# Kernel tuning notes

Measured on AMD Instinct MI355X. Metric: run time of the kernel, lower is better.

## Reference

```python
import jax, jax.numpy as jnp
import numpy as np
from jax import lax

B = 1024
D_VQ = 64
KS = 1024
KX = 1024
BETA = 0.25


def _conv1d(x, w, b):
    # x: [N, Cin, L], w: [Cout, Cin, 3], 'same' padding
    y = lax.conv_general_dilated(x, w, (1,), [(1, 1)], dimension_numbers=('NCH', 'OIH', 'NCH'))
    return y + b[None, :, None]


def _conv2d(x, w, b):
    # x: [N, Cin, H, W], w: [Cout, Cin, 3, 3], 'same' padding
    y = lax.conv_general_dilated(x, w, (1, 1), [(1, 1), (1, 1)], dimension_numbers=('NCHW', 'OIHW', 'NCHW'))
    return y + b[None, :, None, None]


def _gelu(x):
    return jax.nn.gelu(x, approximate=False)


def _vq_ema(z_e, codebook, beta):
    # z_e: [N, D], codebook: [K, D]
    d = (jnp.sum(z_e * z_e, axis=1, keepdims=True)
         - 2.0 * (z_e @ codebook.T)
         + jnp.sum(codebook * codebook, axis=1)[None, :])  # [N, K]
    idx = jnp.argmin(d, axis=1)                              # [N]
    z_q = codebook[idx]                                      # gather [N, D]
    vq_loss = beta * jnp.mean((z_e - lax.stop_gradient(z_q)) ** 2)
    z_q_st = z_e + lax.stop_gradient(z_q - z_e)              # straight-through
    n = z_e.shape[0]
    probs = jnp.zeros((codebook.shape[0],), z_e.dtype).at[idx].add(1.0) / n
    perplexity = jnp.exp(-jnp.sum(probs * jnp.log(probs + 1e-10)))
    return z_q_st, idx, vq_loss, perplexity


def setup_inputs() -> dict:
    key = jax.random.key(0)
    ks = iter(jax.random.split(key, 40))

    def p(shape, s=0.05):
        return jax.random.normal(next(ks), shape, jnp.float32) * s

    inp = {
        'cubes': jax.random.normal(next(ks), (B, 9, 8, 72), jnp.float32),
        # spectral encoder
        's_w1': p((16, 1, 3)), 's_b1': jnp.zeros((16,), jnp.float32),
        's_w2': p((16, 16, 3)), 's_b2': jnp.zeros((16,), jnp.float32),
        's_fc_w': p((D_VQ, 16 * 8)), 's_fc_b': jnp.zeros((D_VQ,), jnp.float32),
        'cb_s': p((KS, D_VQ), 1.0),
        # spectral decoder
        's_dec_fc_w': p((16 * 8, D_VQ)), 's_dec_fc_b': jnp.zeros((16 * 8,), jnp.float32),
        's_dec_w1': p((16, 16, 3)), 's_dec_b1': jnp.zeros((16,), jnp.float32),
        's_dec_w2': p((1, 16, 3)), 's_dec_b2': jnp.zeros((1,), jnp.float32),
        # spatial encoder
        'x_w1': p((16, 8, 3, 3)), 'x_b1': jnp.zeros((16,), jnp.float32),
        'x_w2': p((16, 16, 3, 3)), 'x_b2': jnp.zeros((16,), jnp.float32),
        'x_fc_w': p((D_VQ, 16 * 3 * 3)), 'x_fc_b': jnp.zeros((D_VQ,), jnp.float32),
        'cb_x': p((KX, D_VQ), 1.0),
        # spatial decoder
        'x_dec_fc_w': p((16 * 3 * 3, D_VQ)), 'x_dec_fc_b': jnp.zeros((16 * 3 * 3,), jnp.float32),
        'x_dec_w1': p((16, 16, 3, 3)), 'x_dec_b1': jnp.zeros((16,), jnp.float32),
        'x_dec_w2': p((8, 16, 3, 3)), 'x_dec_b2': jnp.zeros((8,), jnp.float32),
        'return_recon': 1,
    }
    return inp


def reference(cubes, s_w1, s_b1, s_w2, s_b2, s_fc_w, s_fc_b, cb_s,
              s_dec_fc_w, s_dec_fc_b, s_dec_w1, s_dec_b1, s_dec_w2, s_dec_b2,
              x_w1, x_b1, x_w2, x_b2, x_fc_w, x_fc_b, cb_x,
              x_dec_fc_w, x_dec_fc_b, x_dec_w1, x_dec_b1, x_dec_w2, x_dec_b2,
              return_recon):
    b, p, t, f = cubes.shape
    n = b * p * t
    c6 = cubes.reshape(b, p, t, 8, 3, 3)                   # [B,P,T,8,3,3]
    cperm = jnp.transpose(c6, (0, 1, 2, 4, 5, 3))          # [B,P,T,3,3,8]

    # --- spectral path ---
    spec = jnp.mean(cperm, axis=(3, 4))                    # [B,P,T,8]
    spec_seq = spec.reshape(n, 1, 8)
    s = _gelu(_conv1d(spec_seq, s_w1, s_b1))
    s = _gelu(_conv1d(s, s_w2, s_b2))
    z_e_s = s.reshape(n, 16 * 8) @ s_fc_w.T + s_fc_b       # [N,D]
    z_q_s, k_idx, vq_loss_s, perplex_s = _vq_ema(z_e_s, cb_s, BETA)
    emb_s = z_q_s.reshape(b, p, t, D_VQ)
    k_idx = k_idx.reshape(b, p, t)

    # --- spatial path ---
    spatial = c6.reshape(n, 8, 3, 3)
    x = _gelu(_conv2d(spatial, x_w1, x_b1))
    x = _gelu(_conv2d(x, x_w2, x_b2))
    z_e_x = x.reshape(n, 16 * 9) @ x_fc_w.T + x_fc_b
    z_q_x, m_idx, vq_loss_x, perplex_x = _vq_ema(z_e_x, cb_x, BETA)
    emb_x = z_q_x.reshape(b, p, t, D_VQ)
    m_idx = m_idx.reshape(b, p, t)

    total = vq_loss_s + vq_loss_x

    if return_recon:
        s_dec = (z_q_s @ s_dec_fc_w.T + s_dec_fc_b).reshape(n, 16, 8)
        s_dec = _gelu(_conv1d(s_dec, s_dec_w1, s_dec_b1))
        recon_s = _conv1d(s_dec, s_dec_w2, s_dec_b2)[:, 0, :].reshape(b, p, t, 8)
        recon_loss_s = jnp.mean((recon_s - spec) ** 2)

        x_dec = (z_q_x @ x_dec_fc_w.T + x_dec_fc_b).reshape(n, 16, 3, 3)
        x_dec = _gelu(_conv2d(x_dec, x_dec_w1, x_dec_b1))
        recon_x = _conv2d(x_dec, x_dec_w2, x_dec_b2)        # [N,8,3,3]
        recon_loss_x = jnp.mean((recon_x - spatial) ** 2)
        recon_loss_total = recon_loss_s + recon_loss_x
    else:
        recon_loss_total = jnp.float32(0.0)

    return (emb_s, emb_x, k_idx, m_idx, total, perplex_s, perplex_x, recon_loss_total)
```

## Files before the change

### kernel.cpp

```cpp
#include <hip/hip_runtime.h>
#include <math.h>

#define NTOK 73728

__device__ __forceinline__ float gelu_f(float x) {
    return 0.5f * x * (1.0f + erff(x * 0.70710678118654752440f));
}

__global__ void __launch_bounds__(256) k_prep(
    const float* __restrict__ cb_s, const float* __restrict__ cb_x,
    double* __restrict__ cn_s, double* __restrict__ cn_x,
    const float* __restrict__ s_dw1, const float* __restrict__ s_db1,
    const float* __restrict__ s_dfcw, const float* __restrict__ s_dfcb,
    float* __restrict__ weffT_s, float* __restrict__ beff_s,
    const float* __restrict__ x_dw1, const float* __restrict__ x_db1,
    const float* __restrict__ x_dfcw, const float* __restrict__ x_dfcb,
    float* __restrict__ weffT_x, float* __restrict__ beff_x,
    const float* __restrict__ s_fcw, float* __restrict__ fcwT_s,
    const float* __restrict__ x_fcw, float* __restrict__ fcwT_x,
    const float* __restrict__ s_w2, float* __restrict__ sw2T,
    const float* __restrict__ x_w1, float* __restrict__ xw1T,
    const float* __restrict__ x_w2, float* __restrict__ xw2T,
    const float* __restrict__ x_dw2, float* __restrict__ xdw2T)
{
    int bid = blockIdx.x, tid = threadIdx.x;
    if (bid < 8) {
        int i = bid * 256 + tid;
        const float* cb = (i < 1024) ? cb_s : cb_x;
        double* cn = (i < 1024) ? cn_s : cn_x;
        int c = i & 1023;
        double s = 0.0;
        for (int k = 0; k < 64; ++k) { double v = (double)cb[c * 64 + k]; s += v * v; }
        cn[c] = s;
    } else if (bid < 40) {
        int idx = (bid - 8) * 256 + tid;
        int o = idx >> 6, d = idx & 63;
        int c = o >> 3, l = o & 7;
        double acc = 0.0;
        for (int ci = 0; ci < 16; ++ci)
            for (int dd = 0; dd < 3; ++dd) {
                int ll = l + dd - 1;
                if (ll < 0 || ll > 7) continue;
                acc += (double)s_dw1[(c * 16 + ci) * 3 + dd] * (double)s_dfcw[(ci * 8 + ll) * 64 + d];
            }
        weffT_s[d * 132 + o] = (float)acc;
        if (o < 4) weffT_s[d * 132 + 128 + o] = 0.f;
        if (d == 0) {
            double bb = (double)s_db1[c];
            for (int ci = 0; ci < 16; ++ci)
                for (int dd = 0; dd < 3; ++dd) {
                    int ll = l + dd - 1;
                    if (ll < 0 || ll > 7) continue;
                    bb += (double)s_dw1[(c * 16 + ci) * 3 + dd] * (double)s_dfcb[ci * 8 + ll];
                }
            beff_s[o] = (float)bb;
        }
    } else if (bid < 76) {
        int idx = (bid - 40) * 256 + tid;
        int o = idx >> 6, d = idx & 63;
        int c = o / 9, p = o - c * 9;
        int i = p / 3, j = p % 3;
        double acc = 0.0;
        for (int ci = 0; ci < 16; ++ci)
            for (int di = 0; di < 3; ++di) {
                int ii = i + di - 1; if (ii < 0 || ii > 2) continue;
                for (int dj = 0; dj < 3; ++dj) {
                    int jj = j + dj - 1; if (jj < 0 || jj > 2) continue;
                    acc += (double)x_dw1[((c * 16 + ci) * 3 + di) * 3 + dj]
                         * (double)x_dfcw[(ci * 9 + ii * 3 + jj) * 64 + d];
                }
            }
        weffT_x[d * 148 + o] = (float)acc;
        if (o < 4) weffT_x[d * 148 + 144 + o] = 0.f;
        if (d == 0) {
            double bb = (double)x_db1[c];
            for (int ci = 0; ci < 16; ++ci)
                for (int di = 0; di < 3; ++di) {
                    int ii = i + di - 1; if (ii < 0 || ii > 2) continue;
                    for (int dj = 0; dj < 3; ++dj) {
                        int jj = j + dj - 1; if (jj < 0 || jj > 2) continue;
                        bb += (double)x_dw1[((c * 16 + ci) * 3 + di) * 3 + dj]
                            * (double)x_dfcb[ci * 9 + ii * 3 + jj];
                    }
                }
            beff_x[o] = (float)bb;
        }
    } else if (bid < 108) {
        int i = (bid - 76) * 256 + tid;
        fcwT_s[i] = s_fcw[(i & 63) * 128 + (i >> 6)];
    } else if (bid < 144) {
        int i = (bid - 108) * 256 + tid;
        fcwT_x[i] = x_fcw[(i & 63) * 144 + (i >> 6)];
    } else {
        int i = (bid - 144) * 256 + tid;
        if (i < 768) {
            int c = i & 15, r = i >> 4;
            int ci = r / 3, dd = r % 3;
            sw2T[i] = s_w2[(c * 16 + ci) * 3 + dd];
        } else if (i < 1920) {
            int j = i - 768;
            int c = j & 15, r = j >> 4;
            int ci = r / 9, tap = r % 9;
            xw1T[j] = x_w1[(c * 8 + ci) * 9 + tap];
        } else if (i < 4224) {
            int j = i - 1920;
            int c = j & 15, r = j >> 4;
            int ci = r / 9, tap = r % 9;
            xw2T[j] = x_w2[(c * 16 + ci) * 9 + tap];
        } else {
            int j = i - 4224;
            int co = j & 7, r = j >> 3;
            int ci = r / 9, tap = r % 9;
            xdw2T[j] = x_dw2[(co * 16 + ci) * 9 + tap];
        }
    }
}

__global__ void __launch_bounds__(256) k_enc(
    const float* __restrict__ cubes,
    const float* __restrict__ s_w1, const float* __restrict__ s_b1,
    const float* __restrict__ sw2T, const float* __restrict__ s_b2,
    const float* __restrict__ fcwT_s, const float* __restrict__ s_fcb,
    float* __restrict__ emb_s,
    const float* __restrict__ xw1T, const float* __restrict__ x_b1,
    const float* __restrict__ xw2T, const float* __restrict__ x_b2,
    const float* __restrict__ fcwT_x, const float* __restrict__ x_fcb,
    float* __restrict__ emb_x)
{
    __shared__ float U[6528];
    int tid = threadIdx.x;
    int t = tid >> 4, c = tid & 15;
    if (blockIdx.x < 4608) {
        int b = blockIdx.x;
        float* S = U;
        float* A = U + 128;
        float* Bb = U + 2304;
        if (tid < 128) {
            int tk = tid >> 3, f = tid & 7;
            const float* cu = cubes + ((size_t)b * 16 + tk) * 72 + f * 9;
            float s = 0.f;
            #pragma unroll
            for (int k = 0; k < 9; ++k) s += cu[k];
            S[tk * 8 + f] = s * (1.0f / 9.0f);
        }
        __syncthreads();
        {
            float s0[8];
            *(float4*)&s0[0] = *(const float4*)&S[t * 8];
            *(float4*)&s0[4] = *(const float4*)&S[t * 8 + 4];
            float wa = s_w1[c * 3 + 0], wb = s_w1[c * 3 + 1], wc = s_w1[c * 3 + 2], bb = s_b1[c];
            #pragma unroll
            for (int l = 0; l < 8; ++l) {
                float v = fmaf(wb, s0[l], bb);
                if (l > 0) v = fmaf(wa, s0[l - 1], v);
                if (l < 7) v = fmaf(wc, s0[l + 1], v);
                A[t * 136 + c * 8 + l] = gelu_f(v);
            }
        }
        __syncthreads();
        {
            float acc[8];
            #pragma unroll
            for (int l = 0; l < 8; ++l) acc[l] = s_b2[c];
            for (int ci = 0; ci < 16; ++ci) {
                float r[8];
                *(float4*)&r[0] = *(const float4*)&A[t * 136 + ci * 8];
                *(float4*)&r[4] = *(const float4*)&A[t * 136 + ci * 8 + 4];
                float wa = sw2T[(ci * 3 + 0) * 16 + c];
                float wb = sw2T[(ci * 3 + 1) * 16 + c];
                float wc = sw2T[(ci * 3 + 2) * 16 + c];
                #pragma unroll
                for (int l = 0; l < 8; ++l) {
                    if (l > 0) acc[l] = fmaf(wa, r[l - 1], acc[l]);
                    acc[l] = fmaf(wb, r[l], acc[l]);
                    if (l < 7) acc[l] = fmaf(wc, r[l + 1], acc[l]);
                }
            }
            #pragma unroll
            for (int l = 0; l < 8; ++l) Bb[t * 136 + c * 8 + l] = gelu_f(acc[l]);
        }
        __syncthreads();
        {
            float4 zv = make_float4(s_fcb[c * 4 + 0], s_fcb[c * 4 + 1], s_fcb[c * 4 + 2], s_fcb[c * 4 + 3]);
            #pragma unroll 4
            for (int e = 0; e < 128; ++e) {
                float be = Bb[t * 136 + e];
                float4 wv = *(const float4*)(fcwT_s + (e << 6) + (c << 2));
                zv.x = fmaf(wv.x, be, zv.x);
                zv.y = fmaf(wv.y, be, zv.y);
                zv.z = fmaf(wv.z, be, zv.z);
                zv.w = fmaf(wv.w, be, zv.w);
            }
            *(float4*)(emb_s + ((size_t)b * 16 + t) * 64 + c * 4) = zv;
        }
    } else {
        int b = blockIdx.x - 4608;
        float* A = U;
        float* Bb = U + 3200;
        for (int u = tid; u < 1152; u += 256) {
            int tk = u / 72, e = u - tk * 72;
            int ci = e / 9, p = e - ci * 9;
            A[tk * 200 + ci * 12 + p] = cubes[(size_t)b * 1152 + u];
        }
        __syncthreads();
        {
            float acc[9];
            #pragma unroll
            for (int p = 0; p < 9; ++p) acc[p] = x_b1[c];
            for (int ci = 0; ci < 8; ++ci) {
                float r[12];
                *(float4*)&r[0] = *(const float4*)&A[t * 200 + ci * 12];
                *(float4*)&r[4] = *(const float4*)&A[t * 200 + ci * 12 + 4];
                *(float4*)&r[8] = *(const float4*)&A[t * 200 + ci * 12 + 8];
                float wv[9];
                #pragma unroll
                for (int q = 0; q < 9; ++q) wv[q] = xw1T[(ci * 9 + q) * 16 + c];
                #pragma unroll
                for (int p = 0; p < 9; ++p) {
                    int i = p / 3, j = p % 3;
                    #pragma unroll
                    for (int di = 0; di < 3; ++di) {
                        int ii = i + di - 1; if (ii < 0 || ii > 2) continue;
                        #pragma unroll
                        for (int dj = 0; dj < 3; ++dj) {
                            int jj = j + dj - 1; if (jj < 0 || jj > 2) continue;
                            acc[p] = fmaf(wv[di * 3 + dj], r[ii * 3 + jj], acc[p]);
                        }
                    }
                }
            }
            #pragma unroll
            for (int p = 0; p < 9; ++p) Bb[t * 200 + c * 12 + p] = gelu_f(acc[p]);
        }
        __syncthreads();
        {
            float acc[9];
            #pragma unroll
            for (int p = 0; p < 9; ++p) acc[p] = x_b2[c];
            for (int ci = 0; ci < 16; ++ci) {
                float r[12];
                *(float4*)&r[0] = *(const float4*)&Bb[t * 200 + ci * 12];
                *(float4*)&r[4] = *(const float4*)&Bb[t * 200 + ci * 12 + 4];
                *(float4*)&r[8] = *(const float4*)&Bb[t * 200 + ci * 12 + 8];
                float wv[9];
                #pragma unroll
                for (int q = 0; q < 9; ++q) wv[q] = xw2T[(ci * 9 + q) * 16 + c];
                #pragma unroll
                for (int p = 0; p < 9; ++p) {
                    int i = p / 3, j = p % 3;
                    #pragma unroll
                    for (int di = 0; di < 3; ++di) {
                        int ii = i + di - 1; if (ii < 0 || ii > 2) continue;
                        #pragma unroll
                        for (int dj = 0; dj < 3; ++dj) {
                            int jj = j + dj - 1; if (jj < 0 || jj > 2) continue;
                            acc[p] = fmaf(wv[di * 3 + dj], r[ii * 3 + jj], acc[p]);
                        }
                    }
                }
            }
            __syncthreads();
            #pragma unroll
            for (int p = 0; p < 9; ++p) A[t * 200 + c * 12 + p] = gelu_f(acc[p]);
        }
        __syncthreads();
        {
            float4 zv = make_float4(x_fcb[c * 4 + 0], x_fcb[c * 4 + 1], x_fcb[c * 4 + 2], x_fcb[c * 4 + 3]);
            #pragma unroll 4
            for (int e = 0; e < 144; ++e) {
                int ci = e / 9, p = e - ci * 9;
                float be = A[t * 200 + ci * 12 + p];
                float4 wv = *(const float4*)(fcwT_x + (e << 6) + (c << 2));
                zv.x = fmaf(wv.x, be, zv.x);
                zv.y = fmaf(wv.y, be, zv.y);
                zv.z = fmaf(wv.z, be, zv.z);
                zv.w = fmaf(wv.w, be, zv.w);
            }
            *(float4*)(emb_x + ((size_t)b * 16 + t) * 64 + c * 4) = zv;
        }
    }
}

__global__ void __launch_bounds__(256) k_vq(
    float* __restrict__ emb_s, float* __restrict__ emb_x,
    const float* __restrict__ cb_s, const float* __restrict__ cb_x,
    const double* __restrict__ cn_s, const double* __restrict__ cn_x,
    float* __restrict__ kidx, float* __restrict__ midx,
    int* __restrict__ hist_s, int* __restrict__ hist_x,
    double* __restrict__ p_vq_s, double* __restrict__ p_vq_x)
{
    __shared__ double pbest[4][64];
    __shared__ int pidx[4][64];
    __shared__ int lh[1024];
    int blk = blockIdx.x;
    int path = (blk >= 1152) ? 1 : 0;
    int b = blk - (path << 10) - (path << 7);
    float* emb = path ? emb_x : emb_s;
    const float* cb = path ? cb_x : cb_s;
    const double* cn = path ? cn_x : cn_s;
    float* idx_out = path ? midx : kidx;
    int* hist = path ? hist_x : hist_s;
    double* partial = path ? p_vq_x : p_vq_s;

    int tid = threadIdx.x;
    int w = tid >> 6, l = tid & 63;
    for (int u = tid; u < 1024; u += 256) lh[u] = 0;
    size_t n = (size_t)b * 64 + l;
    float z[64];
    {
        const float4* zp = (const float4*)(emb + n * 64);
        #pragma unroll
        for (int k = 0; k < 16; ++k) *(float4*)&z[k * 4] = zp[k];
    }
    int base = __builtin_amdgcn_readfirstlane(w << 8);
    const float* crb = cb + ((size_t)base << 6);
    const double* cnb = cn + base;
    double best = 1e300; int bi = base;
    for (int cc = 0; cc < 256; ++cc) {
        const float* cr = crb + (cc << 6);
        float d0 = 0.f, d1 = 0.f, d2 = 0.f, d3 = 0.f;
        #pragma unroll
        for (int k = 0; k < 64; k += 4) {
            d0 = fmaf(z[k + 0], cr[k + 0], d0);
            d1 = fmaf(z[k + 1], cr[k + 1], d1);
            d2 = fmaf(z[k + 2], cr[k + 2], d2);
            d3 = fmaf(z[k + 3], cr[k + 3], d3);
        }
        float dot = (d0 + d1) + (d2 + d3);
        double dd = cnb[cc] - 2.0 * (double)dot;
        if (dd < best) { best = dd; bi = base + cc; }
    }
    pbest[w][l] = best; pidx[w][l] = bi;
    __syncthreads();
    if (w == 0) {
        double bB = pbest[0][l]; int bj = pidx[0][l];
        #pragma unroll
        for (int q = 1; q < 4; ++q) {
            double d = pbest[q][l];
            if (d < bB) { bB = d; bj = pidx[q][l]; }
        }
        idx_out[n] = (float)bj;
        float qv[64];
        {
            const float4* cq = (const float4*)(cb + ((size_t)bj << 6));
            #pragma unroll
            for (int k = 0; k < 16; ++k) *(float4*)&qv[k * 4] = cq[k];
        }
        float vs = 0.f;
        #pragma unroll
        for (int k = 0; k < 64; ++k) { float df = z[k] - qv[k]; vs = fmaf(df, df, vs); }
        float4* zo = (float4*)(emb + n * 64);
        #pragma unroll
        for (int k = 0; k < 16; ++k) zo[k] = *(float4*)&qv[k * 4];
        atomicAdd(&lh[bj], 1);
        double s = (double)vs;
        #pragma unroll
        for (int o = 32; o > 0; o >>= 1) s += __shfl_down(s, o);
        if (l == 0) partial[b] = s;
    }
    __syncthreads();
    for (int u = tid; u < 1024; u += 256) if (lh[u] > 0) atomicAdd(&hist[u], lh[u]);
}

__global__ void __launch_bounds__(256) k_dec(
    const float* __restrict__ emb_s, const float* __restrict__ emb_x,
    const float* __restrict__ cubes,
    const float* __restrict__ weffT_s, const float* __restrict__ beff_s,
    const float* __restrict__ s_dw2, const float* __restrict__ s_db2,
    const float* __restrict__ weffT_x, const float* __restrict__ beff_x,
    const float* __restrict__ xdw2T, const float* __restrict__ x_db2,
    double* __restrict__ p_rec_s, double* __restrict__ p_rec_x)
{
    __shared__ float U[6016];
    __shared__ double wred[4];
    int tid = threadIdx.x;
    int t = tid >> 4, c = tid & 15;
    if (blockIdx.x < 4608) {
        int b = blockIdx.x;
        float* Z = U;
        float* Bb = U + 1152;
        float* S = U + 3328;
        {
            int tk = tid >> 4, dq = tid & 15;
            *(float4*)&Z[tk * 72 + dq * 4] =
                *(const float4*)(emb_s + (size_t)b * 1024 + (size_t)tid * 4);
        }
        if (tid < 128) {
            int tk = tid >> 3, f = tid & 7;
            const float* cu = cubes + ((size_t)b * 16 + tk) * 72 + f * 9;
            float s = 0.f;
            #pragma unroll
            for (int k = 0; k < 9; ++k) s += cu[k];
            S[tk * 8 + f] = s * (1.0f / 9.0f);
        }
        __syncthreads();
        {
            float4 a0 = make_float4(0.f, 0.f, 0.f, 0.f);
            float4 a1 = make_float4(0.f, 0.f, 0.f, 0.f);
            #pragma unroll 8
            for (int k = 0; k < 64; ++k) {
                float zk = Z[t * 72 + k];
                float4 w0 = *(const float4*)(weffT_s + k * 132 + (c << 2));
                float4 w1v = *(const float4*)(weffT_s + k * 132 + 64 + (c << 2));
                a0.x = fmaf(w0.x, zk, a0.x); a0.y = fmaf(w0.y, zk, a0.y);
                a0.z = fmaf(w0.z, zk, a0.z); a0.w = fmaf(w0.w, zk, a0.w);
                a1.x = fmaf(w1v.x, zk, a1.x); a1.y = fmaf(w1v.y, zk, a1.y);
                a1.z = fmaf(w1v.z, zk, a1.z); a1.w = fmaf(w1v.w, zk, a1.w);
            }
            int o0 = c << 2, o1 = 64 + (c << 2);
            float4 g0 = make_float4(gelu_f(a0.x + beff_s[o0 + 0]), gelu_f(a0.y + beff_s[o0 + 1]),
                                    gelu_f(a0.z + beff_s[o0 + 2]), gelu_f(a0.w + beff_s[o0 + 3]));
            float4 g1 = make_float4(gelu_f(a1.x + beff_s[o1 + 0]), gelu_f(a1.y + beff_s[o1 + 1]),
                                    gelu_f(a1.z + beff_s[o1 + 2]), gelu_f(a1.w + beff_s[o1 + 3]));
            *(float4*)&Bb[t * 136 + o0] = g0;
            *(float4*)&Bb[t * 136 + o1] = g1;
        }
        __syncthreads();
        float acc2 = 0.f;
        {
            int h = c >> 3, pos = c & 7;
            float a = (h == 0) ? s_db2[0] : 0.f;
            for (int ci = h * 8; ci < h * 8 + 8; ++ci) {
                const float* w = s_dw2 + ci * 3;
                const float* hb = &Bb[t * 136 + ci * 8];
                if (pos > 0) a = fmaf(w[0], hb[pos - 1], a);
                a = fmaf(w[1], hb[pos], a);
                if (pos < 7) a = fmaf(w[2], hb[pos + 1], a);
            }
            a += __shfl_xor(a, 8);
            if (h == 0) { float df = a - S[t * 8 + pos]; acc2 = df * df; }
        }
        double s = (double)acc2;
        #pragma unroll
        for (int o = 32; o > 0; o >>= 1) s += __shfl_down(s, o);
        if ((tid & 63) == 0) wred[tid >> 6] = s;
        __syncthreads();
        if (tid == 0) p_rec_s[b] = wred[0] + wred[1] + wred[2] + wred[3];
    } else {
        int b = blockIdx.x - 4608;
        float* Z = U;
        float* H = U + 1152;
        float* T = U + 4352;
        {
            int tk = tid >> 4, dq = tid & 15;
            *(float4*)&Z[tk * 72 + dq * 4] =
                *(const float4*)(emb_x + (size_t)b * 1024 + (size_t)tid * 4);
        }
        for (int u = tid; u < 1152; u += 256) {
            int tk = u / 72, e = u - tk * 72;
            int ci = e / 9, p = e - ci * 9;
            T[tk * 104 + ci * 12 + p] = cubes[(size_t)b * 1152 + u];
        }
        __syncthreads();
        {
            float4 a0 = make_float4(0.f, 0.f, 0.f, 0.f);
            float4 a1 = make_float4(0.f, 0.f, 0.f, 0.f);
            float4 a2 = make_float4(0.f, 0.f, 0.f, 0.f);
            #pragma unroll 8
            for (int k = 0; k < 64; ++k) {
                float zk = Z[t * 72 + k];
                float4 w0 = *(const float4*)(weffT_x + k * 148 + (c << 2));
                float4 w1v = *(const float4*)(weffT_x + k * 148 + 64 + (c << 2));
                float4 w2v = *(const float4*)(weffT_x + k * 148 + 128 + (c << 2));
                a0.x = fmaf(w0.x, zk, a0.x); a0.y = fmaf(w0.y, zk, a0.y);
                a0.z = fmaf(w0.z, zk, a0.z); a0.w = fmaf(w0.w, zk, a0.w);
                a1.x = fmaf(w1v.x, zk, a1.x); a1.y = fmaf(w1v.y, zk, a1.y);
                a1.z = fmaf(w1v.z, zk, a1.z); a1.w = fmaf(w1v.w, zk, a1.w);
                a2.x = fmaf(w2v.x, zk, a2.x); a2.y = fmaf(w2v.y, zk, a2.y);
                a2.z = fmaf(w2v.z, zk, a2.z); a2.w = fmaf(w2v.w, zk, a2.w);
            }
            float av[12] = {a0.x, a0.y, a0.z, a0.w, a1.x, a1.y, a1.z, a1.w, a2.x, a2.y, a2.z, a2.w};
            #pragma unroll
            for (int q = 0; q < 12; ++q) {
                int o = (c << 2) + ((q >> 2) << 6) + (q & 3);
                int ch = o / 9, p = o - ch * 9;
                H[t * 200 + ch * 12 + p] = gelu_f(av[q] + beff_x[o]);
            }
        }
        __syncthreads();
        float acc2 = 0.f;
        {
            int co = c >> 1, h = c & 1;
            float accp[9];
            #pragma unroll
            for (int p = 0; p < 9; ++p) accp[p] = (h == 0) ? x_db2[co] : 0.f;
            for (int ci = h * 8; ci < h * 8 + 8; ++ci) {
                float r[12];
                *(float4*)&r[0] = *(const float4*)&H[t * 200 + ci * 12];
                *(float4*)&r[4] = *(const float4*)&H[t * 200 + ci * 12 + 4];
                *(float4*)&r[8] = *(const float4*)&H[t * 200 + ci * 12 + 8];
                float wv[9];
                #pragma unroll
                for (int q = 0; q < 9; ++q) wv[q] = xdw2T[(ci * 9 + q) * 8 + co];
                #pragma unroll
                for (int p = 0; p < 9; ++p) {
                    int i = p / 3, j = p % 3;
                    #pragma unroll
                    for (int di = 0; di < 3; ++di) {
                        int ii = i + di - 1; if (ii < 0 || ii > 2) continue;
                        #pragma unroll
                        for (int dj = 0; dj < 3; ++dj) {
                            int jj = j + dj - 1; if (jj < 0 || jj > 2) continue;
                            accp[p] = fmaf(wv[di * 3 + dj], r[ii * 3 + jj], accp[p]);
                        }
                    }
                }
            }
            #pragma unroll
            for (int p = 0; p < 9; ++p) {
                float tot = accp[p] + __shfl_xor(accp[p], 1);
                if (h == 0) { float df = tot - T[t * 104 + co * 12 + p]; acc2 = fmaf(df, df, acc2); }
            }
        }
        double s = (double)acc2;
        #pragma unroll
        for (int o = 32; o > 0; o >>= 1) s += __shfl_down(s, o);
        if ((tid & 63) == 0) wred[tid >> 6] = s;
        __syncthreads();
        if (tid == 0) p_rec_x[b] = wred[0] + wred[1] + wred[2] + wred[3];
    }
}

__global__ void __launch_bounds__(256) k_final(
    const double* __restrict__ p_vq_s, const double* __restrict__ p_vq_x,
    const double* __restrict__ p_rec_s, const double* __restrict__ p_rec_x,
    const int* __restrict__ hist_s, const int* __restrict__ hist_x,
    const int* __restrict__ rr,
    float* __restrict__ outscal)
{
    __shared__ double wred[4];
    int tid = threadIdx.x;
    auto bred = [&](double v) -> double {
        #pragma unroll
        for (int o = 32; o > 0; o >>= 1) v += __shfl_down(v, o);
        __syncthreads();
        if ((tid & 63) == 0) wred[tid >> 6] = v;
        __syncthreads();
        return wred[0] + wred[1] + wred[2] + wred[3];
    };
    double a;
    a = 0; for (int t = tid; t < 1152; t += 256) a += p_vq_s[t];
    double vq_s = bred(a);
    a = 0; for (int t = tid; t < 1152; t += 256) a += p_vq_x[t];
    double vq_x = bred(a);
    a = 0; for (int t = tid; t < 4608; t += 256) a += p_rec_s[t];
    double rec_s = bred(a);
    a = 0; for (int t = tid; t < 4608; t += 256) a += p_rec_x[t];
    double rec_x = bred(a);
    a = 0;
    for (int t = tid; t < 1024; t += 256) {
        double cnt = (double)hist_s[t];
        if (cnt > 0.0) { double p = cnt / (double)NTOK; a += p * log(p + 1e-10); }
    }
    double ent_s = bred(a);
    a = 0;
    for (int t = tid; t < 1024; t += 256) {
        double cnt = (double)hist_x[t];
        if (cnt > 0.0) { double p = cnt / (double)NTOK; a += p * log(p + 1e-10); }
    }
    double ent_x = bred(a);
    if (tid == 0) {
        double total = 0.25 * (vq_s / 4718592.0 + vq_x / 4718592.0);
        double rec = (rr[0] != 0) ? (rec_s / 589824.0 + rec_x / 5308416.0) : 0.0;
        outscal[0] = (float)total;
        outscal[1] = (float)exp(-ent_s);
        outscal[2] = (float)exp(-ent_x);
        outscal[3] = (float)rec;
    }
}

extern "C" void kernel_launch(void* const* d_in, const int* in_sizes, int n_in,
                              void* d_out, int out_size, void* d_ws, size_t ws_size,
                              hipStream_t stream)
{
    const float* cubes  = (const float*)d_in[0];
    const float* s_w1   = (const float*)d_in[1];
    const float* s_b1   = (const float*)d_in[2];
    const float* s_w2   = (const float*)d_in[3];
    const float* s_b2   = (const float*)d_in[4];
    const float* s_fcw  = (const float*)d_in[5];
    const float* s_fcb  = (const float*)d_in[6];
    const float* cb_s   = (const float*)d_in[7];
    const float* s_dfcw = (const float*)d_in[8];
    const float* s_dfcb = (const float*)d_in[9];
    const float* s_dw1  = (const float*)d_in[10];
    const float* s_db1  = (const float*)d_in[11];
    const float* s_dw2  = (const float*)d_in[12];
    const float* s_db2  = (const float*)d_in[13];
    const float* x_w1   = (const float*)d_in[14];
    const float* x_b1   = (const float*)d_in[15];
    const float* x_w2   = (const float*)d_in[16];
    const float* x_b2   = (const float*)d_in[17];
    const float* x_fcw  = (const float*)d_in[18];
    const float* x_fcb  = (const float*)d_in[19];
    const float* cb_x   = (const float*)d_in[20];
    const float* x_dfcw = (const float*)d_in[21];
    const float* x_dfcb = (const float*)d_in[22];
    const float* x_dw1  = (const float*)d_in[23];
    const float* x_db1  = (const float*)d_in[24];
    const float* x_dw2  = (const float*)d_in[25];
    const float* x_db2  = (const float*)d_in[26];
    const int*   rr     = (const int*)d_in[27];

    float* out   = (float*)d_out;
    float* emb_s = out;
    float* emb_x = out + 4718592;
    float* kidx  = out + 9437184;
    float* midx  = out + 9510912;
    float* scal  = out + 9584640;

    char* ws = (char*)d_ws;
    int*    hist_s  = (int*)(ws + 0);
    int*    hist_x  = (int*)(ws + 4096);
    double* cn_s    = (double*)(ws + 8192);
    double* cn_x    = (double*)(ws + 16384);
    double* p_vq_s  = (double*)(ws + 24576);
    double* p_vq_x  = (double*)(ws + 33792);
    double* p_rec_s = (double*)(ws + 43008);
    double* p_rec_x = (double*)(ws + 79872);
    float*  beff_s  = (float*)(ws + 116736);
    float*  beff_x  = (float*)(ws + 117248);
    float*  weffT_s = (float*)(ws + 117824);
    float*  weffT_x = (float*)(ws + 151616);
    float*  fcwT_s  = (float*)(ws + 189504);
    float*  fcwT_x  = (float*)(ws + 222272);
    float*  sw2T    = (float*)(ws + 259136);
    float*  xw1T    = (float*)(ws + 262208);
    float*  xw2T    = (float*)(ws + 266816);
    float*  xdw2T   = (float*)(ws + 276032);

    hipMemsetAsync(d_ws, 0, 8192, stream);
    k_prep<<<165, 256, 0, stream>>>(cb_s, cb_x, cn_s, cn_x,
                                    s_dw1, s_db1, s_dfcw, s_dfcb, weffT_s, beff_s,
                                    x_dw1, x_db1, x_dfcw, x_dfcb, weffT_x, beff_x,
                                    s_fcw, fcwT_s, x_fcw, fcwT_x,
                                    s_w2, sw2T, x_w1, xw1T, x_w2, xw2T, x_dw2, xdw2T);
    k_enc<<<9216, 256, 0, stream>>>(cubes, s_w1, s_b1, sw2T, s_b2, fcwT_s, s_fcb, emb_s,
                                    xw1T, x_b1, xw2T, x_b2, fcwT_x, x_fcb, emb_x);
    k_vq<<<2304, 256, 0, stream>>>(emb_s, emb_x, cb_s, cb_x, cn_s, cn_x,
                                   kidx, midx, hist_s, hist_x, p_vq_s, p_vq_x);
    k_dec<<<9216, 256, 0, stream>>>(emb_s, emb_x, cubes,
                                    weffT_s, beff_s, s_dw2, s_db2,
                                    weffT_x, beff_x, xdw2T, x_db2,
                                    p_rec_s, p_rec_x);
    k_final<<<1, 256, 0, stream>>>(p_vq_s, p_vq_x, p_rec_s, p_rec_x, hist_s, hist_x, rr, scal);
}
```

Measured before the change: 883.1 us.

## Process two tokens per thread in VQ search to reuse codebook loads

Each thread in the VQ argmin kernel now scores two tokens against the same codebook rows, so every codebook load is shared by twice as many FMAs. The grid is halved and per-block partial loss storage and the final reduction are adjusted to match. The cost is higher register pressure from two 64-float token vectors, which may lower occupancy, and fewer blocks to spread across the GPU.

```diff
diff --git a/kernel.cpp b/kernel.cpp
--- a/kernel.cpp
+++ b/kernel.cpp
@@ -289,12 +289,13 @@
     int* __restrict__ hist_s, int* __restrict__ hist_x,
     double* __restrict__ p_vq_s, double* __restrict__ p_vq_x)
 {
-    __shared__ double pbest[4][64];
-    __shared__ int pidx[4][64];
+    __shared__ double pbest[4][128];
+    __shared__ int pidx[4][128];
     __shared__ int lh[1024];
+    __shared__ double wred2[2];
     int blk = blockIdx.x;
-    int path = (blk >= 1152) ? 1 : 0;
-    int b = blk - (path << 10) - (path << 7);
+    int path = (blk >= 576) ? 1 : 0;
+    int b = blk - path * 576;
     float* emb = path ? emb_x : emb_s;
     const float* cb = path ? cb_x : cb_s;
     const double* cn = path ? cn_x : cn_s;
@@ -305,60 +306,90 @@
     int tid = threadIdx.x;
     int w = tid >> 6, l = tid & 63;
     for (int u = tid; u < 1024; u += 256) lh[u] = 0;
-    size_t n = (size_t)b * 64 + l;
-    float z[64];
+    size_t n1 = (size_t)b * 128 + l;
+    float z1[64], z2[64];
     {
-        const float4* zp = (const float4*)(emb + n * 64);
+        const float4* zp1 = (const float4*)(emb + n1 * 64);
+        const float4* zp2 = (const float4*)(emb + (n1 + 64) * 64);
         #pragma unroll
-        for (int k = 0; k < 16; ++k) *(float4*)&z[k * 4] = zp[k];
+        for (int k = 0; k < 16; ++k) {
+            *(float4*)&z1[k * 4] = zp1[k];
+            *(float4*)&z2[k * 4] = zp2[k];
+        }
     }
     int base = __builtin_amdgcn_readfirstlane(w << 8);
     const float* crb = cb + ((size_t)base << 6);
     const double* cnb = cn + base;
-    double best = 1e300; int bi = base;
+    double best1 = 1e300, best2 = 1e300; int bi1 = base, bi2 = base;
     for (int cc = 0; cc < 256; ++cc) {
         const float* cr = crb + (cc << 6);
-        float d0 = 0.f, d1 = 0.f, d2 = 0.f, d3 = 0.f;
+        float a0 = 0.f, a1 = 0.f, a2 = 0.f, a3 = 0.f;
+        float e0 = 0.f, e1 = 0.f, e2 = 0.f, e3 = 0.f;
         #pragma unroll
         for (int k = 0; k < 64; k += 4) {
-            d0 = fmaf(z[k + 0], cr[k + 0], d0);
-            d1 = fmaf(z[k + 1], cr[k + 1], d1);
-            d2 = fmaf(z[k + 2], cr[k + 2], d2);
-            d3 = fmaf(z[k + 3], cr[k + 3], d3);
-        }
-        float dot = (d0 + d1) + (d2 + d3);
-        double dd = cnb[cc] - 2.0 * (double)dot;
-        if (dd < best) { best = dd; bi = base + cc; }
-    }
-    pbest[w][l] = best; pidx[w][l] = bi;
+            float c0 = cr[k + 0], c1 = cr[k + 1], c2 = cr[k + 2], c3 = cr[k + 3];
+            a0 = fmaf(z1[k + 0], c0, a0);
+            a1 = fmaf(z1[k + 1], c1, a1);
+            a2 = fmaf(z1[k + 2], c2, a2);
+            a3 = fmaf(z1[k + 3], c3, a3);
+            e0 = fmaf(z2[k + 0], c0, e0);
+            e1 = fmaf(z2[k + 1], c1, e1);
+            e2 = fmaf(z2[k + 2], c2, e2);
+            e3 = fmaf(z2[k + 3], c3, e3);
+        }
+        float dot1 = (a0 + a1) + (a2 + a3);
+        float dot2 = (e0 + e1) + (e2 + e3);
+        double cnv = cnb[cc];
+        double dd1 = cnv - 2.0 * (double)dot1;
+        double dd2 = cnv - 2.0 * (double)dot2;
+        if (dd1 < best1) { best1 = dd1; bi1 = base + cc; }
+        if (dd2 < best2) { best2 = dd2; bi2 = base + cc; }
+    }
+    pbest[w][l] = best1;      pidx[w][l] = bi1;
+    pbest[w][64 + l] = best2; pidx[w][64 + l] = bi2;
     __syncthreads();
-    if (w == 0) {
-        double bB = pbest[0][l]; int bj = pidx[0][l];
+    if (w < 2) {
+        int tl = (w << 6) + l;
+        double bB = pbest[0][tl]; int bj = pidx[0][tl];
         #pragma unroll
         for (int q = 1; q < 4; ++q) {
-            double d = pbest[q][l];
-            if (d < bB) { bB = d; bj = pidx[q][l]; }
-        }
+            double d = pbest[q][tl];
+            if (d < bB) { bB = d; bj = pidx[q][tl]; }
+        }
+        size_t n = (size_t)b * 128 + tl;
         idx_out[n] = (float)bj;
-        float qv[64];
-        {
-            const float4* cq = (const float4*)(cb + ((size_t)bj << 6));
-            #pragma unroll
-            for (int k = 0; k < 16; ++k) *(float4*)&qv[k * 4] = cq[k];
-        }
+        atomicAdd(&lh[bj], 1);
+        const float4* cq = (const float4*)(cb + ((size_t)bj << 6));
+        float4* zo = (float4*)(emb + n * 64);
         float vs = 0.f;
-        #pragma unroll
-        for (int k = 0; k < 64; ++k) { float df = z[k] - qv[k]; vs = fmaf(df, df, vs); }
-        float4* zo = (float4*)(emb + n * 64);
-        #pragma unroll
-        for (int k = 0; k < 16; ++k) zo[k] = *(float4*)&qv[k * 4];
-        atomicAdd(&lh[bj], 1);
+        if (w == 0) {
+            #pragma unroll
+            for (int r = 0; r < 16; ++r) {
+                float4 qv = cq[r];
+                float dx = z1[r * 4 + 0] - qv.x, dy = z1[r * 4 + 1] - qv.y;
+                float dz = z1[r * 4 + 2] - qv.z, dw = z1[r * 4 + 3] - qv.w;
+                vs = fmaf(dx, dx, vs); vs = fmaf(dy, dy, vs);
+                vs = fmaf(dz, dz, vs); vs = fmaf(dw, dw, vs);
+                zo[r] = qv;
+            }
+        } else {
+            #pragma unroll
+            for (int r = 0; r < 16; ++r) {
+                float4 qv = cq[r];
+                float dx = z2[r * 4 + 0] - qv.x, dy = z2[r * 4 + 1] - qv.y;
+                float dz = z2[r * 4 + 2] - qv.z, dw = z2[r * 4 + 3] - qv.w;
+                vs = fmaf(dx, dx, vs); vs = fmaf(dy, dy, vs);
+                vs = fmaf(dz, dz, vs); vs = fmaf(dw, dw, vs);
+                zo[r] = qv;
+            }
+        }
         double s = (double)vs;
         #pragma unroll
         for (int o = 32; o > 0; o >>= 1) s += __shfl_down(s, o);
-        if (l == 0) partial[b] = s;
+        if (l == 0) wred2[w] = s;
     }
     __syncthreads();
+    if (tid == 0) partial[b] = wred2[0] + wred2[1];
     for (int u = tid; u < 1024; u += 256) if (lh[u] > 0) atomicAdd(&hist[u], lh[u]);
 }
 
@@ -539,9 +570,9 @@
         return wred[0] + wred[1] + wred[2] + wred[3];
     };
     double a;
-    a = 0; for (int t = tid; t < 1152; t += 256) a += p_vq_s[t];
+    a = 0; for (int t = tid; t < 576; t += 256) a += p_vq_s[t];
     double vq_s = bred(a);
-    a = 0; for (int t = tid; t < 1152; t += 256) a += p_vq_x[t];
+    a = 0; for (int t = tid; t < 576; t += 256) a += p_vq_x[t];
     double vq_x = bred(a);
     a = 0; for (int t = tid; t < 4608; t += 256) a += p_rec_s[t];
     double rec_s = bred(a);
@@ -637,7 +668,7 @@
                                     s_w2, sw2T, x_w1, xw1T, x_w2, xw2T, x_dw2, xdw2T);
     k_enc<<<9216, 256, 0, stream>>>(cubes, s_w1, s_b1, sw2T, s_b2, fcwT_s, s_fcb, emb_s,
                                     xw1T, x_b1, xw2T, x_b2, fcwT_x, x_fcb, emb_x);
-    k_vq<<<2304, 256, 0, stream>>>(emb_s, emb_x, cb_s, cb_x, cn_s, cn_x,
+    k_vq<<<1152, 256, 0, stream>>>(emb_s, emb_x, cb_s, cb_x, cn_s, cn_x,
                                    kidx, midx, hist_s, hist_x, p_vq_s, p_vq_x);
     k_dec<<<9216, 256, 0, stream>>>(emb_s, emb_x, cubes,
                                     weffT_s, beff_s, s_dw2, s_db2,
```

Result: slower. 1.318 ms (+49.2%).
